# Performance work log

Hardware: AMD Instinct MI355X
Metric: run time of the kernel (lower is better)

The kernel has to match this reference:

```python
import jax, jax.numpy as jnp
import numpy as np

DIM = 512
HEADS = 2
DIM_HEAD = 64          # dim // 8
INNER = HEADS * DIM_HEAD
M = 256                # num_landmarks = dim // 2
PINV_ITERS = 6
KERNEL = 33            # residual_conv_kernel default
LN_EPS = 1e-5


def setup_inputs() -> dict:
    key = jax.random.key(0)
    ks = jax.random.split(key, 5)
    b, n = 4, 8192
    x = jax.random.normal(ks[0], (b, n, DIM), jnp.float32)
    gamma = jnp.ones((DIM,), jnp.float32)
    beta = jnp.zeros((DIM,), jnp.float32)
    w_qkv = jax.random.normal(ks[1], (DIM, 3 * INNER), jnp.float32) * 0.02
    w_out = jax.random.normal(ks[2], (INNER, DIM), jnp.float32) * 0.02
    b_out = jnp.zeros((DIM,), jnp.float32)
    w_res = jax.random.normal(ks[3], (HEADS, 1, KERNEL, 1), jnp.float32) * 0.02
    return {"x": x, "gamma": gamma, "beta": beta, "w_qkv": w_qkv,
            "w_out": w_out, "b_out": b_out, "w_res": w_res}


def moore_penrose_pinv(x, iters=PINV_ITERS):
    # x: [b, h, m, m]
    abs_x = jnp.abs(x)
    col = abs_x.sum(-1)
    row = abs_x.sum(-2)
    z = jnp.swapaxes(x, -1, -2) / (jnp.max(col) * jnp.max(row))
    I = jnp.eye(x.shape[-1], dtype=x.dtype)
    for _ in range(iters):
        xz = x @ z
        z = 0.25 * z @ (13 * I - xz @ (15 * I - xz @ (7 * I - xz)))
    return z


def reference(x, gamma, beta, w_qkv, w_out, b_out, w_res):
    b, n, d = x.shape
    # LayerNorm
    mu = x.mean(-1, keepdims=True)
    var = jnp.mean((x - mu) ** 2, axis=-1, keepdims=True)
    xn = (x - mu) / jnp.sqrt(var + LN_EPS) * gamma + beta
    # pad seq (on the left) to a multiple of M; no-op when n % M == 0
    rem = n % M
    if rem:
        xn = jnp.pad(xn, ((0, 0), (M - rem, 0), (0, 0)))
    N = xn.shape[1]
    qkv = xn @ w_qkv                        # [b, N, 3*INNER]
    q, k, v = jnp.split(qkv, 3, axis=-1)
    to_heads = lambda t: t.reshape(b, N, HEADS, DIM_HEAD).transpose(0, 2, 1, 3)
    q, k, v = to_heads(q), to_heads(k), to_heads(v)   # [b, h, N, dh]
    q = q * (DIM_HEAD ** -0.5)
    l = N // M
    q_l = q.reshape(b, HEADS, M, l, DIM_HEAD).mean(3)  # [b, h, M, dh]
    k_l = k.reshape(b, HEADS, M, l, DIM_HEAD).mean(3)
    sim1 = jnp.einsum('bhid,bhjd->bhij', q, k_l)       # [b, h, N, M]
    sim2 = jnp.einsum('bhid,bhjd->bhij', q_l, k_l)     # [b, h, M, M]
    sim3 = jnp.einsum('bhid,bhjd->bhij', q_l, k)       # [b, h, M, N]
    a1 = jax.nn.softmax(sim1, axis=-1)
    a2 = jax.nn.softmax(sim2, axis=-1)
    a3 = jax.nn.softmax(sim3, axis=-1)
    a2_inv = moore_penrose_pinv(a2)
    out = (a1 @ a2_inv) @ (a3 @ v)                     # [b, h, N, dh]
    # depthwise residual conv over sequence dim of v
    res = jax.lax.conv_general_dilated(
        v, w_res, window_strides=(1, 1),
        padding=[(KERNEL // 2, KERNEL // 2), (0, 0)],
        dimension_numbers=('NCHW', 'OIHW', 'NCHW'),
        feature_group_count=HEADS)
    out = out + res
    out = out.transpose(0, 2, 1, 3).reshape(b, N, INNER)
    out = out @ w_out + b_out
    out = out[:, -n:]
    return x + out
```

## Files before the change

kernel.cpp:

```cpp
#include <hip/hip_runtime.h>
#include <math.h>


#define BB 4
#define HH 2
#define NSEQ 8192
#define DMODEL 512
#define DH 64
#define MLAND 256
#define LCH 32
#define W3 384
#define INNER 128
#define KER 33
#define BH (BB*HH)

typedef __attribute__((ext_vector_type(8))) short short8v;
typedef __attribute__((ext_vector_type(4))) short short4v;
typedef __attribute__((ext_vector_type(4))) float f32x4;

__device__ __forceinline__ short f2bf(float f) {
    unsigned u = __float_as_uint(f);
    u = (u + 0x7FFFu + ((u >> 16) & 1u)) >> 16;
    return (short)u;
}

__global__ __launch_bounds__(256) void ln_qkv_kernel(
    const float* __restrict__ x, const float* __restrict__ gamma,
    const float* __restrict__ beta, const float* __restrict__ wqkv,
    float* __restrict__ q, float* __restrict__ k, float* __restrict__ v)
{
    __shared__ float xn[32][513];
    __shared__ float gs[512];
    __shared__ float bs[512];
    const int t = threadIdx.x;
    const int row0 = blockIdx.x * 32;

    for (int i = t; i < 512; i += 256) { gs[i] = gamma[i]; bs[i] = beta[i]; }
    __syncthreads();

    const int wave = t >> 6;
    const int lane = t & 63;
    #pragma unroll 1
    for (int i = 0; i < 8; ++i) {
        const int r = wave * 8 + i;
        const float* xr = x + (size_t)(row0 + r) * DMODEL + lane * 8;
        const float4 a = *(const float4*)(xr);
        const float4 b = *(const float4*)(xr + 4);
        float s  = a.x + a.y + a.z + a.w + b.x + b.y + b.z + b.w;
        float ss = a.x*a.x + a.y*a.y + a.z*a.z + a.w*a.w
                 + b.x*b.x + b.y*b.y + b.z*b.z + b.w*b.w;
        #pragma unroll
        for (int o = 32; o > 0; o >>= 1) {
            s  += __shfl_xor(s, o, 64);
            ss += __shfl_xor(ss, o, 64);
        }
        const float mu = s * (1.0f/512.0f);
        const float var = ss * (1.0f/512.0f) - mu*mu;
        const float rstd = rsqrtf(var + 1e-5f);
        const int c = lane * 8;
        xn[r][c+0] = (a.x - mu) * rstd * gs[c+0] + bs[c+0];
        xn[r][c+1] = (a.y - mu) * rstd * gs[c+1] + bs[c+1];
        xn[r][c+2] = (a.z - mu) * rstd * gs[c+2] + bs[c+2];
        xn[r][c+3] = (a.w - mu) * rstd * gs[c+3] + bs[c+3];
        xn[r][c+4] = (b.x - mu) * rstd * gs[c+4] + bs[c+4];
        xn[r][c+5] = (b.y - mu) * rstd * gs[c+5] + bs[c+5];
        xn[r][c+6] = (b.z - mu) * rstd * gs[c+6] + bs[c+6];
        xn[r][c+7] = (b.w - mu) * rstd * gs[c+7] + bs[c+7];
    }
    __syncthreads();

    const int c0 = (t & 63) * 6;
    const int r0 = (t >> 6) * 8;
    float acc[8][6];
    #pragma unroll
    for (int i = 0; i < 8; ++i)
        #pragma unroll
        for (int j = 0; j < 6; ++j) acc[i][j] = 0.0f;

    #pragma unroll 4
    for (int kk = 0; kk < 512; ++kk) {
        const float* wrow = wqkv + (size_t)kk * W3 + c0;
        const float w0 = wrow[0], w1 = wrow[1], w2 = wrow[2];
        const float w3 = wrow[3], w4 = wrow[4], w5 = wrow[5];
        #pragma unroll
        for (int i = 0; i < 8; ++i) {
            const float xv = xn[r0+i][kk];
            acc[i][0] = fmaf(xv, w0, acc[i][0]);
            acc[i][1] = fmaf(xv, w1, acc[i][1]);
            acc[i][2] = fmaf(xv, w2, acc[i][2]);
            acc[i][3] = fmaf(xv, w3, acc[i][3]);
            acc[i][4] = fmaf(xv, w4, acc[i][4]);
            acc[i][5] = fmaf(xv, w5, acc[i][5]);
        }
    }

    #pragma unroll
    for (int i = 0; i < 8; ++i) {
        const int grow = row0 + r0 + i;
        const int b = grow >> 13;
        const int n = grow & (NSEQ - 1);
        #pragma unroll
        for (int j = 0; j < 6; ++j) {
            const int c = c0 + j;
            const float val = acc[i][j];
            if (c < INNER) {
                const int h = c >> 6, d = c & 63;
                q[(((size_t)b*HH + h)*NSEQ + n)*DH + d] = val * 0.125f;
            } else if (c < 2*INNER) {
                const int cc = c - INNER;
                const int h = cc >> 6, d = cc & 63;
                k[(((size_t)b*HH + h)*NSEQ + n)*DH + d] = val;
            } else {
                const int cc = c - 2*INNER;
                const int h = cc >> 6, d = cc & 63;
                v[(((size_t)b*HH + h)*NSEQ + n)*DH + d] = val;
            }
        }
    }
}

__global__ __launch_bounds__(256) void landmark_kernel(
    const float* __restrict__ q, const float* __restrict__ k,
    float* __restrict__ ql, float* __restrict__ kl)
{
    const int t = threadIdx.x;
    const int g = blockIdx.x * 4 + (t >> 6);
    const int d = t & 63;
    const int bh = g >> 8;
    const int m  = g & 255;
    const float* qb = q + ((size_t)bh * NSEQ + (size_t)m * LCH) * DH + d;
    const float* kb = k + ((size_t)bh * NSEQ + (size_t)m * LCH) * DH + d;
    float sq = 0.0f, sk = 0.0f;
    #pragma unroll
    for (int i = 0; i < LCH; ++i) { sq += qb[i*DH]; sk += kb[i*DH]; }
    ql[((size_t)bh * MLAND + m) * DH + d] = sq * (1.0f/LCH);
    kl[((size_t)bh * MLAND + m) * DH + d] = sk * (1.0f/LCH);
}

__global__ __launch_bounds__(256) void sim2_kernel(
    const float* __restrict__ ql, const float* __restrict__ kl,
    float* __restrict__ a2)
{
    const int bh = blockIdx.x >> 8;
    const int i  = blockIdx.x & 255;
    const int j  = threadIdx.x;
    __shared__ float qrow[64];
    __shared__ float red[8];
    if (j < 64) qrow[j] = ql[((size_t)bh*MLAND + i)*DH + j];
    __syncthreads();
    const float4* k4 = (const float4*)(kl + ((size_t)bh*MLAND + j)*DH);
    float s = 0.0f;
    #pragma unroll
    for (int u = 0; u < 16; ++u) {
        const float4 kv = k4[u];
        s = fmaf(qrow[u*4+0], kv.x, s);
        s = fmaf(qrow[u*4+1], kv.y, s);
        s = fmaf(qrow[u*4+2], kv.z, s);
        s = fmaf(qrow[u*4+3], kv.w, s);
    }
    float m = s;
    #pragma unroll
    for (int o = 32; o > 0; o >>= 1) m = fmaxf(m, __shfl_xor(m, o, 64));
    if ((j & 63) == 0) red[j >> 6] = m;
    __syncthreads();
    m = fmaxf(fmaxf(red[0], red[1]), fmaxf(red[2], red[3]));
    const float e = __expf(s - m);
    float l = e;
    #pragma unroll
    for (int o = 32; o > 0; o >>= 1) l += __shfl_xor(l, o, 64);
    if ((j & 63) == 0) red[4 + (j >> 6)] = l;
    __syncthreads();
    l = red[4] + red[5] + red[6] + red[7];
    a2[((size_t)bh*MLAND + i)*MLAND + j] = e / l;
}

__global__ void initmax_kernel(unsigned int* mx) {
    if (threadIdx.x < 2) mx[threadIdx.x] = 0u;
}

__global__ __launch_bounds__(256) void pinv_sums_kernel(
    const float* __restrict__ a2, unsigned int* __restrict__ mx)
{
    const int bh = blockIdx.x;
    const int t = threadIdx.x;
    const float* A = a2 + (size_t)bh * MLAND * MLAND;
    float rs = 0.0f, cs = 0.0f;
    const float4* row4 = (const float4*)(A + (size_t)t * MLAND);
    #pragma unroll 8
    for (int u = 0; u < 64; ++u) {
        const float4 val = row4[u];
        rs += fabsf(val.x) + fabsf(val.y) + fabsf(val.z) + fabsf(val.w);
    }
    #pragma unroll 8
    for (int i = 0; i < MLAND; ++i) cs += fabsf(A[(size_t)i*MLAND + t]);
    __shared__ float red[8];
    float mrs = rs, mcs = cs;
    #pragma unroll
    for (int o = 32; o > 0; o >>= 1) {
        mrs = fmaxf(mrs, __shfl_xor(mrs, o, 64));
        mcs = fmaxf(mcs, __shfl_xor(mcs, o, 64));
    }
    if ((t & 63) == 0) { red[t>>6] = mrs; red[4+(t>>6)] = mcs; }
    __syncthreads();
    if (t == 0) {
        const float a = fmaxf(fmaxf(red[0],red[1]), fmaxf(red[2],red[3]));
        const float b = fmaxf(fmaxf(red[4],red[5]), fmaxf(red[6],red[7]));
        atomicMax(&mx[0], __float_as_uint(a));
        atomicMax(&mx[1], __float_as_uint(b));
    }
}

__global__ __launch_bounds__(256) void z0_kernel(
    const float* __restrict__ a2, const unsigned int* __restrict__ mx,
    float* __restrict__ z)
{
    const float scale = 1.0f / (__uint_as_float(mx[0]) * __uint_as_float(mx[1]));
    const size_t idx = (size_t)blockIdx.x * 256 + threadIdx.x;
    const size_t bh = idx >> 16;
    const size_t i = (idx >> 8) & 255;
    const size_t j = idx & 255;
    z[idx] = a2[(bh << 16) | (j << 8) | i] * scale;
}

__global__ __launch_bounds__(256) void mm256_kernel(
    float* __restrict__ C, const float* __restrict__ A,
    const float* __restrict__ Bm, float c1, float c2, int NC)
{
    __shared__ float As[32][65];
    __shared__ float Bs[64][68];
    const int bh = blockIdx.z;
    const int row0 = blockIdx.y * 32;
    const int col0 = blockIdx.x * 64;
    const float* Ab = A + (size_t)bh * MLAND * MLAND;
    const float* Bb = Bm + (size_t)bh * MLAND * NC;
    const int t = threadIdx.x;
    const int tc = (t & 15) * 4;
    const int tr = (t >> 4) * 2;
    float acc[2][4] = {{0,0,0,0},{0,0,0,0}};
    for (int k0 = 0; k0 < 256; k0 += 64) {
        #pragma unroll
        for (int u = 0; u < 2; ++u) {
            const int idx = t + u*256;
            const int r = idx >> 4, c4 = (idx & 15) * 4;
            const float4 val = *(const float4*)(Ab + (size_t)(row0 + r) * MLAND + k0 + c4);
            As[r][c4+0] = val.x; As[r][c4+1] = val.y;
            As[r][c4+2] = val.z; As[r][c4+3] = val.w;
        }
        #pragma unroll
        for (int u = 0; u < 4; ++u) {
            const int idx = t + u*256;
            const int r = idx >> 4, c4 = (idx & 15) * 4;
            *(float4*)&Bs[r][c4] = *(const float4*)(Bb + (size_t)(k0 + r) * NC + col0 + c4);
        }
        __syncthreads();
        #pragma unroll 8
        for (int kk = 0; kk < 64; ++kk) {
            const float a0 = As[tr][kk];
            const float a1 = As[tr+1][kk];
            const float4 b4 = *(const float4*)&Bs[kk][tc];
            acc[0][0] = fmaf(a0, b4.x, acc[0][0]);
            acc[0][1] = fmaf(a0, b4.y, acc[0][1]);
            acc[0][2] = fmaf(a0, b4.z, acc[0][2]);
            acc[0][3] = fmaf(a0, b4.w, acc[0][3]);
            acc[1][0] = fmaf(a1, b4.x, acc[1][0]);
            acc[1][1] = fmaf(a1, b4.y, acc[1][1]);
            acc[1][2] = fmaf(a1, b4.z, acc[1][2]);
            acc[1][3] = fmaf(a1, b4.w, acc[1][3]);
        }
        __syncthreads();
    }
    #pragma unroll
    for (int i = 0; i < 2; ++i) {
        const int r = row0 + tr + i;
        #pragma unroll
        for (int j = 0; j < 4; ++j) {
            const int c = col0 + tc + j;
            float val = c2 * acc[i][j];
            if (c1 != 0.0f) val = fmaf(c1, Ab[(size_t)r * MLAND + c], val);
            C[((size_t)bh * MLAND + r) * NC + c] = val;
        }
    }
}

__global__ __launch_bounds__(256, 1) void sim3_kernel(
    const float* __restrict__ ql, const float* __restrict__ kg,
    const float* __restrict__ vg, float* __restrict__ po,
    float* __restrict__ pm, float* __restrict__ pl)
{
    __shared__ float ks[64][68];
    __shared__ float vs[64][68];
    const int ch = blockIdx.x;
    const int bh = blockIdx.y;
    const int t = threadIdx.x;
    float4 q4[16];
    {
        const float* qr = ql + ((size_t)bh * MLAND + t) * DH;
        #pragma unroll
        for (int u = 0; u < 16; ++u) q4[u] = *(const float4*)(qr + u*4);
    }
    float4 o4[16];
    #pragma unroll
    for (int u = 0; u < 16; ++u) o4[u] = make_float4(0.f,0.f,0.f,0.f);
    float m = -1e30f, l = 0.0f;

    #pragma unroll 1
    for (int sc = 0; sc < 4; ++sc) {
        const int j0 = ch * 256 + sc * 64;
        #pragma unroll
        for (int u = 0; u < 4; ++u) {
            const int idx = t + u*256;
            const int r = idx >> 4, c4 = (idx & 15) * 4;
            *(float4*)&ks[r][c4] = *(const float4*)(kg + ((size_t)bh*NSEQ + j0 + r)*DH + c4);
            *(float4*)&vs[r][c4] = *(const float4*)(vg + ((size_t)bh*NSEQ + j0 + r)*DH + c4);
        }
        __syncthreads();
        #pragma unroll 1
        for (int b16 = 0; b16 < 4; ++b16) {
            float s[16];
            #pragma unroll
            for (int c = 0; c < 16; ++c) {
                const int cc = b16*16 + c;
                float a = 0.0f;
                #pragma unroll
                for (int u = 0; u < 16; ++u) {
                    const float4 kv = *(const float4*)&ks[cc][u*4];
                    a = fmaf(q4[u].x, kv.x, a);
                    a = fmaf(q4[u].y, kv.y, a);
                    a = fmaf(q4[u].z, kv.z, a);
                    a = fmaf(q4[u].w, kv.w, a);
                }
                s[c] = a;
            }
            float bm = s[0];
            #pragma unroll
            for (int c = 1; c < 16; ++c) bm = fmaxf(bm, s[c]);
            const float mn = fmaxf(m, bm);
            const float scale = __expf(m - mn);
            l *= scale;
            #pragma unroll
            for (int u = 0; u < 16; ++u) {
                o4[u].x *= scale; o4[u].y *= scale;
                o4[u].z *= scale; o4[u].w *= scale;
            }
            #pragma unroll
            for (int c = 0; c < 16; ++c) {
                const int cc = b16*16 + c;
                const float p = __expf(s[c] - mn);
                l += p;
                #pragma unroll
                for (int u = 0; u < 16; ++u) {
                    const float4 vv = *(const float4*)&vs[cc][u*4];
                    o4[u].x = fmaf(p, vv.x, o4[u].x);
                    o4[u].y = fmaf(p, vv.y, o4[u].y);
                    o4[u].z = fmaf(p, vv.z, o4[u].z);
                    o4[u].w = fmaf(p, vv.w, o4[u].w);
                }
            }
            m = mn;
        }
        __syncthreads();
    }
    float* od = po + (((size_t)bh*32 + ch) * MLAND + t) * DH;
    #pragma unroll
    for (int u = 0; u < 16; ++u) *(float4*)(od + u*4) = o4[u];
    pm[((size_t)bh*32 + ch) * MLAND + t] = m;
    pl[((size_t)bh*32 + ch) * MLAND + t] = l;
}

__global__ __launch_bounds__(256) void sim3red_kernel(
    const float* __restrict__ po, const float* __restrict__ pm,
    const float* __restrict__ pl, float* __restrict__ a3v)
{
    const int g = blockIdx.x * 4 + (threadIdx.x >> 6);
    const int d = threadIdx.x & 63;
    const int bh = g >> 8;
    const int r = g & 255;
    float M = -1e30f;
    #pragma unroll
    for (int c = 0; c < 32; ++c)
        M = fmaxf(M, pm[((size_t)bh*32 + c)*MLAND + r]);
    float L = 0.0f, o = 0.0f;
    #pragma unroll 1
    for (int c = 0; c < 32; ++c) {
        const float w = __expf(pm[((size_t)bh*32 + c)*MLAND + r] - M);
        L = fmaf(pl[((size_t)bh*32 + c)*MLAND + r], w, L);
        o = fmaf(po[(((size_t)bh*32 + c)*MLAND + r)*DH + d], w, o);
    }
    a3v[((size_t)bh*MLAND + r)*DH + d] = o / L;
}

__global__ __launch_bounds__(256) void packkl_kernel(
    const float* __restrict__ klm, short* __restrict__ klb)
{
    const int idx = blockIdx.x * 256 + threadIdx.x;
    klb[idx] = f2bf(klm[idx]);
}

__global__ __launch_bounds__(256) void packwt_kernel(
    const float* __restrict__ Wm, short* __restrict__ wtb)
{
    const int idx = blockIdx.x * 256 + threadIdx.x;
    const int bh = idx >> 14;
    const int rem = idx & 16383;
    const int d = rem >> 8;
    const int m = rem & 255;
    wtb[idx] = f2bf(Wm[((size_t)bh * MLAND + m) * DH + d]);
}

__global__ __launch_bounds__(256, 2) void final1_mfma_kernel(
    const float* __restrict__ q, const short* __restrict__ klb,
    const short* __restrict__ wtb, float* __restrict__ inner)
{
    __shared__ short ldsA[16384];
    __shared__ short ldsW[16384];
    const int bh = blockIdx.y;
    const int b = bh >> 1;
    const int h = bh & 1;
    const int t = threadIdx.x;
    const int w = t >> 6;
    const int l = t & 63;
    const int lr = l & 15;
    const int lg = l >> 4;

    {
        const short* klsrc = klb + (size_t)bh * 16384;
        const short* wtsrc = wtb + (size_t)bh * 16384;
        #pragma unroll
        for (int u = 0; u < 8; ++u) {
            const int gi = t + u * 256;
            const int m  = gi >> 3, sl = gi & 7;
            *(short8v*)&ldsA[m*64 + (sl ^ (m & 7))*8] =
                *(const short8v*)(klsrc + gi*8);
            const int dd = gi >> 5, sw = gi & 31;
            *(short8v*)&ldsW[dd*256 + (sw ^ (dd & 7))*8] =
                *(const short8v*)(wtsrc + gi*8);
        }
    }
    __syncthreads();

    const int n = blockIdx.x * 64 + w * 16 + lr;
    short8v qb0, qb1;
    {
        const float* qr = q + ((size_t)bh * NSEQ + n) * DH + lg * 8;
        const float4 f0 = *(const float4*)qr;
        const float4 f1 = *(const float4*)(qr + 4);
        const float4 f2 = *(const float4*)(qr + 32);
        const float4 f3 = *(const float4*)(qr + 36);
        qb0[0]=f2bf(f0.x); qb0[1]=f2bf(f0.y); qb0[2]=f2bf(f0.z); qb0[3]=f2bf(f0.w);
        qb0[4]=f2bf(f1.x); qb0[5]=f2bf(f1.y); qb0[6]=f2bf(f1.z); qb0[7]=f2bf(f1.w);
        qb1[0]=f2bf(f2.x); qb1[1]=f2bf(f2.y); qb1[2]=f2bf(f2.z); qb1[3]=f2bf(f2.w);
        qb1[4]=f2bf(f3.x); qb1[5]=f2bf(f3.y); qb1[6]=f2bf(f3.z); qb1[7]=f2bf(f3.w);
    }

    f32x4 accS[16];
    #pragma unroll
    for (int mt = 0; mt < 16; ++mt) accS[mt] = (f32x4){0.f,0.f,0.f,0.f};
    const int s8 = lr & 7;
    #pragma unroll
    for (int mt = 0; mt < 16; ++mt) {
        const int m = mt * 16 + lr;
        const short8v a0 = *(const short8v*)&ldsA[m*64 + ((0*4 + lg) ^ s8)*8];
        const short8v a1 = *(const short8v*)&ldsA[m*64 + ((1*4 + lg) ^ s8)*8];
        accS[mt] = __builtin_amdgcn_mfma_f32_16x16x32_bf16(a0, qb0, accS[mt], 0, 0, 0);
        accS[mt] = __builtin_amdgcn_mfma_f32_16x16x32_bf16(a1, qb1, accS[mt], 0, 0, 0);
    }

    float mloc = -1e30f;
    #pragma unroll
    for (int mt = 0; mt < 16; ++mt)
        #pragma unroll
        for (int j = 0; j < 4; ++j) mloc = fmaxf(mloc, accS[mt][j]);
    mloc = fmaxf(mloc, __shfl_xor(mloc, 16, 64));
    mloc = fmaxf(mloc, __shfl_xor(mloc, 32, 64));
    float lsum = 0.0f;
    #pragma unroll
    for (int mt = 0; mt < 16; ++mt)
        #pragma unroll
        for (int j = 0; j < 4; ++j) {
            const float p = __expf(accS[mt][j] - mloc);
            accS[mt][j] = p;
            lsum += p;
        }
    lsum += __shfl_xor(lsum, 16, 64);
    lsum += __shfl_xor(lsum, 32, 64);

    __syncthreads();

    {
        short* pw = ldsA + w * 4096;
        #pragma unroll
        for (int mt = 0; mt < 16; ++mt) {
            short4v pk;
            pk[0] = f2bf(accS[mt][0]); pk[1] = f2bf(accS[mt][1]);
            pk[2] = f2bf(accS[mt][2]); pk[3] = f2bf(accS[mt][3]);
            const int byteoff = (mt*32 + lg*8) ^ (s8 << 4);
            *(short4v*)&pw[lr*256 + (byteoff >> 1)] = pk;
        }
    }
    __syncthreads();

    short8v pb[8];
    {
        const short* pw = ldsA + w * 4096;
        #pragma unroll
        for (int kc = 0; kc < 8; ++kc) {
            const int byteoff = (kc*64 + lg*16) ^ (s8 << 4);
            pb[kc] = *(const short8v*)&pw[lr*256 + (byteoff >> 1)];
        }
    }
    f32x4 accO[4];
    #pragma unroll
    for (int dt = 0; dt < 4; ++dt) accO[dt] = (f32x4){0.f,0.f,0.f,0.f};
    #pragma unroll
    for (int dt = 0; dt < 4; ++dt) {
        const int d = dt * 16 + lr;
        #pragma unroll
        for (int kc = 0; kc < 8; ++kc) {
            const short8v wa = *(const short8v*)&ldsW[d*256 + (((kc*64 + lg*16) ^ (s8 << 4)) >> 1)];
            accO[dt] = __builtin_amdgcn_mfma_f32_16x16x32_bf16(wa, pb[kc], accO[dt], 0, 0, 0);
        }
    }

    const float rl = 1.0f / lsum;
    float* ob = inner + ((size_t)b * NSEQ + n) * INNER + h * DH + lg * 4;
    #pragma unroll
    for (int dt = 0; dt < 4; ++dt) {
        float4 o;
        o.x = accO[dt][0] * rl; o.y = accO[dt][1] * rl;
        o.z = accO[dt][2] * rl; o.w = accO[dt][3] * rl;
        *(float4*)(ob + dt * 16) = o;
    }
}

__global__ __launch_bounds__(256) void conv_add_kernel(
    const float* __restrict__ vg, const float* __restrict__ wres,
    float* __restrict__ inner)
{
    __shared__ float wr[KER];
    const int bh = blockIdx.y;
    const int b = bh >> 1;
    const int h = bh & 1;
    const int t = threadIdx.x;
    if (t < KER) wr[t] = wres[h*KER + t];
    __syncthreads();
    const int d = t & 63;
    const int g = t >> 6;
    const int n0 = blockIdx.x * 128;
    #pragma unroll 1
    for (int i = 0; i < 32; ++i) {
        const int n = n0 + g + i*4;
        float acc = 0.0f;
        #pragma unroll
        for (int tt = 0; tt < KER; ++tt) {
            const int nn = n - 16 + tt;
            if (nn >= 0 && nn < NSEQ)
                acc = fmaf(vg[((size_t)bh*NSEQ + nn)*DH + d], wr[tt], acc);
        }
        const size_t idx = ((size_t)b*NSEQ + n)*INNER + h*DH + d;
        inner[idx] += acc;
    }
}

__global__ __launch_bounds__(256) void final2_kernel(
    const float* __restrict__ inner, const float* __restrict__ wout,
    const float* __restrict__ bout, const float* __restrict__ x,
    float* __restrict__ out)
{
    __shared__ float is[32][129];
    const int t = threadIdx.x;
    const size_t row0 = (size_t)blockIdx.x * 32;
    #pragma unroll
    for (int u = 0; u < 4; ++u) {
        const int idx = t + u*256;
        const int r = idx >> 5, c4 = (idx & 31) * 4;
        const float4 val = *(const float4*)(inner + (row0 + r)*INNER + c4);
        is[r][c4+0]=val.x; is[r][c4+1]=val.y; is[r][c4+2]=val.z; is[r][c4+3]=val.w;
    }
    __syncthreads();
    const int c0 = (t & 63) * 8;
    const int r0 = (t >> 6) * 8;
    float acc[8][8];
    #pragma unroll
    for (int i = 0; i < 8; ++i)
        #pragma unroll
        for (int j = 0; j < 8; ++j) acc[i][j] = 0.0f;
    #pragma unroll 2
    for (int kk = 0; kk < 128; ++kk) {
        const float4 w0 = *(const float4*)(wout + (size_t)kk*DMODEL + c0);
        const float4 w1 = *(const float4*)(wout + (size_t)kk*DMODEL + c0 + 4);
        #pragma unroll
        for (int i = 0; i < 8; ++i) {
            const float xv = is[r0+i][kk];
            acc[i][0] = fmaf(xv, w0.x, acc[i][0]);
            acc[i][1] = fmaf(xv, w0.y, acc[i][1]);
            acc[i][2] = fmaf(xv, w0.z, acc[i][2]);
            acc[i][3] = fmaf(xv, w0.w, acc[i][3]);
            acc[i][4] = fmaf(xv, w1.x, acc[i][4]);
            acc[i][5] = fmaf(xv, w1.y, acc[i][5]);
            acc[i][6] = fmaf(xv, w1.z, acc[i][6]);
            acc[i][7] = fmaf(xv, w1.w, acc[i][7]);
        }
    }
    const float4 b0 = *(const float4*)(bout + c0);
    const float4 b1 = *(const float4*)(bout + c0 + 4);
    #pragma unroll
    for (int i = 0; i < 8; ++i) {
        const size_t row = row0 + r0 + i;
        const float4 x0 = *(const float4*)(x + row*DMODEL + c0);
        const float4 x1 = *(const float4*)(x + row*DMODEL + c0 + 4);
        float4 o0, o1;
        o0.x = acc[i][0] + b0.x + x0.x;
        o0.y = acc[i][1] + b0.y + x0.y;
        o0.z = acc[i][2] + b0.z + x0.z;
        o0.w = acc[i][3] + b0.w + x0.w;
        o1.x = acc[i][4] + b1.x + x1.x;
        o1.y = acc[i][5] + b1.y + x1.y;
        o1.z = acc[i][6] + b1.z + x1.z;
        o1.w = acc[i][7] + b1.w + x1.w;
        *(float4*)(out + row*DMODEL + c0) = o0;
        *(float4*)(out + row*DMODEL + c0 + 4) = o1;
    }
}

extern "C" void kernel_launch(void* const* d_in, const int* in_sizes, int n_in,
                              void* d_out, int out_size, void* d_ws, size_t ws_size,
                              hipStream_t stream)
{
    const float* x     = (const float*)d_in[0];
    const float* gamma = (const float*)d_in[1];
    const float* beta  = (const float*)d_in[2];
    const float* wqkv  = (const float*)d_in[3];
    const float* wout  = (const float*)d_in[4];
    const float* bout  = (const float*)d_in[5];
    const float* wres  = (const float*)d_in[6];
    float* out = (float*)d_out;

    float* ws = (float*)d_ws;
    const size_t QS = (size_t)BH * NSEQ * DH;
    const size_t LS = (size_t)BH * MLAND * DH;
    const size_t MS = (size_t)BH * MLAND * MLAND;
    float* q    = ws;
    float* kbuf = q + QS;
    float* vbuf = kbuf + QS;
    float* ql   = vbuf + QS;
    float* klm  = ql + LS;
    float* a2   = klm + LS;
    float* zA   = a2 + MS;
    float* zB   = zA + MS;
    float* xz   = zB + MS;
    float* t1   = xz + MS;
    float* t2   = t1 + MS;
    float* a3v  = t2 + MS;
    float* Wm   = a3v + LS;
    float* po   = Wm + LS;
    float* pm   = po + QS;
    float* pl   = pm + (size_t)BH * 32 * MLAND;
    unsigned int* mx = (unsigned int*)(pl + (size_t)BH * 32 * MLAND);
    float* inner = po;
    short* klb = (short*)kbuf;
    short* wtb = (short*)kbuf + LS;

    ln_qkv_kernel<<<(BB*NSEQ)/32, 256, 0, stream>>>(x, gamma, beta, wqkv, q, kbuf, vbuf);
    landmark_kernel<<<(BH*MLAND)/4, 256, 0, stream>>>(q, kbuf, ql, klm);
    sim2_kernel<<<BH*MLAND, 256, 0, stream>>>(ql, klm, a2);

    sim3_kernel<<<dim3(32, BH), 256, 0, stream>>>(ql, kbuf, vbuf, po, pm, pl);
    sim3red_kernel<<<(BH*MLAND)/4, 256, 0, stream>>>(po, pm, pl, a3v);

    initmax_kernel<<<1, 64, 0, stream>>>(mx);
    pinv_sums_kernel<<<BH, 256, 0, stream>>>(a2, mx);
    z0_kernel<<<(unsigned)(MS/256), 256, 0, stream>>>(a2, mx, zA);
    float* za = zA;
    float* zb = zB;
    for (int it = 0; it < 6; ++it) {
        mm256_kernel<<<dim3(4,8,BH), 256, 0, stream>>>(xz, a2, za, 0.0f, 1.0f, 256);
        mm256_kernel<<<dim3(4,8,BH), 256, 0, stream>>>(t1, xz, xz, 7.0f, -1.0f, 256);
        mm256_kernel<<<dim3(4,8,BH), 256, 0, stream>>>(t2, xz, t1, 15.0f, -1.0f, 256);
        mm256_kernel<<<dim3(4,8,BH), 256, 0, stream>>>(zb, za, t2, 3.25f, -0.25f, 256);
        float* tmp = za; za = zb; zb = tmp;
    }
    mm256_kernel<<<dim3(1,8,BH), 256, 0, stream>>>(Wm, za, a3v, 0.0f, 1.0f, 64);

    packkl_kernel<<<(unsigned)(LS/256), 256, 0, stream>>>(klm, klb);
    packwt_kernel<<<(unsigned)(LS/256), 256, 0, stream>>>(Wm, wtb);

    final1_mfma_kernel<<<dim3(NSEQ/64, BH), 256, 0, stream>>>(q, klb, wtb, inner);
    conv_add_kernel<<<dim3(NSEQ/128, BH), 256, 0, stream>>>(vbuf, wres, inner);
    final2_kernel<<<(BB*NSEQ)/32, 256, 0, stream>>>(inner, wout, bout, x, out);
}
```

Baseline: 1.129 ms.

## Move QKV and output projections to bf16 MFMA with packed weight fragments

```diff
diff --git a/kernel.cpp b/kernel.cpp
--- a/kernel.cpp
+++ b/kernel.cpp
@@ -24,26 +24,75 @@
     return (short)u;
 }
 
-__global__ __launch_bounds__(256) void ln_qkv_kernel(
+__device__ __forceinline__ void gload_lds16(const short* g, short* l) {
+    __builtin_amdgcn_global_load_lds(
+        (const __attribute__((address_space(1))) unsigned int*)(g),
+        (__attribute__((address_space(3))) unsigned int*)(l), 16, 0, 0);
+}
+
+__global__ __launch_bounds__(256) void pack_wqkv_kernel(
+    const float* __restrict__ w, short* __restrict__ wf)
+{
+    const int idx = blockIdx.x * 256 + threadIdx.x;
+    const int l = idx & 63;
+    const int ct = (idx >> 6) % 24;
+    const int ks = idx / 1536;
+    const int c = ct * 16 + (l & 15);
+    const int k0 = ks * 32 + (l >> 4) * 8;
+    short8v o;
+    #pragma unroll
+    for (int j = 0; j < 8; ++j) o[j] = f2bf(w[(size_t)(k0 + j) * W3 + c]);
+    *(short8v*)&wf[(size_t)idx * 8] = o;
+}
+
+__global__ __launch_bounds__(256) void pack_wout_kernel(
+    const float* __restrict__ w, short* __restrict__ wf)
+{
+    const int idx = blockIdx.x * 256 + threadIdx.x;
+    const int l = idx & 63;
+    const int ct = (idx >> 6) & 31;
+    const int ks = idx >> 11;
+    const int c = ct * 16 + (l & 15);
+    const int k0 = ks * 32 + (l >> 4) * 8;
+    short8v o;
+    #pragma unroll
+    for (int j = 0; j < 8; ++j) o[j] = f2bf(w[(size_t)(k0 + j) * DMODEL + c]);
+    *(short8v*)&wf[(size_t)idx * 8] = o;
+}
+
+__global__ __launch_bounds__(256) void pack_inner_kernel(
+    const float* __restrict__ in, short* __restrict__ o)
+{
+    const size_t i8 = (size_t)blockIdx.x * 256 + threadIdx.x;
+    const float4 a = *(const float4*)(in + i8 * 8);
+    const float4 b = *(const float4*)(in + i8 * 8 + 4);
+    short8v s;
+    s[0]=f2bf(a.x); s[1]=f2bf(a.y); s[2]=f2bf(a.z); s[3]=f2bf(a.w);
+    s[4]=f2bf(b.x); s[5]=f2bf(b.y); s[6]=f2bf(b.z); s[7]=f2bf(b.w);
+    *(short8v*)&o[i8 * 8] = s;
+}
+
+__global__ __launch_bounds__(256, 1) void ln_qkv_mfma_kernel(
     const float* __restrict__ x, const float* __restrict__ gamma,
-    const float* __restrict__ beta, const float* __restrict__ wqkv,
+    const float* __restrict__ beta, const short* __restrict__ wfrag,
     float* __restrict__ q, float* __restrict__ k, float* __restrict__ v)
 {
-    __shared__ float xn[32][513];
+    __shared__ short xn[64 * 512];
+    __shared__ short bsh[2 * 12288];
     __shared__ float gs[512];
-    __shared__ float bs[512];
+    __shared__ float bs2[512];
     const int t = threadIdx.x;
-    const int row0 = blockIdx.x * 32;
-
-    for (int i = t; i < 512; i += 256) { gs[i] = gamma[i]; bs[i] = beta[i]; }
-    __syncthreads();
-
-    const int wave = t >> 6;
+    const int w = t >> 6;
     const int lane = t & 63;
+    const int row0 = blockIdx.x * 64;
+
+    for (int i = t; i < 512; i += 256) { gs[i] = gamma[i]; bs2[i] = beta[i]; }
+    __syncthreads();
+
     #pragma unroll 1
-    for (int i = 0; i < 8; ++i) {
-        const int r = wave * 8 + i;
-        const float* xr = x + (size_t)(row0 + r) * DMODEL + lane * 8;
+    for (int i = 0; i < 16; ++i) {
+        const int r = w * 16 + i;
+        const float* xr = x + ((size_t)row0 + r) * DMODEL + lane * 8;
         const float4 a = *(const float4*)(xr);
         const float4 b = *(const float4*)(xr + 4);
         float s  = a.x + a.y + a.z + a.w + b.x + b.y + b.z + b.w;
@@ -58,63 +107,68 @@
         const float var = ss * (1.0f/512.0f) - mu*mu;
         const float rstd = rsqrtf(var + 1e-5f);
         const int c = lane * 8;
-        xn[r][c+0] = (a.x - mu) * rstd * gs[c+0] + bs[c+0];
-        xn[r][c+1] = (a.y - mu) * rstd * gs[c+1] + bs[c+1];
-        xn[r][c+2] = (a.z - mu) * rstd * gs[c+2] + bs[c+2];
-        xn[r][c+3] = (a.w - mu) * rstd * gs[c+3] + bs[c+3];
-        xn[r][c+4] = (b.x - mu) * rstd * gs[c+4] + bs[c+4];
-        xn[r][c+5] = (b.y - mu) * rstd * gs[c+5] + bs[c+5];
-        xn[r][c+6] = (b.z - mu) * rstd * gs[c+6] + bs[c+6];
-        xn[r][c+7] = (b.w - mu) * rstd * gs[c+7] + bs[c+7];
-    }
-    __syncthreads();
-
-    const int c0 = (t & 63) * 6;
-    const int r0 = (t >> 6) * 8;
-    float acc[8][6];
-    #pragma unroll
-    for (int i = 0; i < 8; ++i)
-        #pragma unroll
-        for (int j = 0; j < 6; ++j) acc[i][j] = 0.0f;
-
-    #pragma unroll 4
-    for (int kk = 0; kk < 512; ++kk) {
-        const float* wrow = wqkv + (size_t)kk * W3 + c0;
-        const float w0 = wrow[0], w1 = wrow[1], w2 = wrow[2];
-        const float w3 = wrow[3], w4 = wrow[4], w5 = wrow[5];
-        #pragma unroll
-        for (int i = 0; i < 8; ++i) {
-            const float xv = xn[r0+i][kk];
-            acc[i][0] = fmaf(xv, w0, acc[i][0]);
-            acc[i][1] = fmaf(xv, w1, acc[i][1]);
-            acc[i][2] = fmaf(xv, w2, acc[i][2]);
-            acc[i][3] = fmaf(xv, w3, acc[i][3]);
-            acc[i][4] = fmaf(xv, w4, acc[i][4]);
-            acc[i][5] = fmaf(xv, w5, acc[i][5]);
-        }
-    }
-
-    #pragma unroll
-    for (int i = 0; i < 8; ++i) {
-        const int grow = row0 + r0 + i;
-        const int b = grow >> 13;
-        const int n = grow & (NSEQ - 1);
-        #pragma unroll
-        for (int j = 0; j < 6; ++j) {
-            const int c = c0 + j;
-            const float val = acc[i][j];
-            if (c < INNER) {
-                const int h = c >> 6, d = c & 63;
-                q[(((size_t)b*HH + h)*NSEQ + n)*DH + d] = val * 0.125f;
-            } else if (c < 2*INNER) {
-                const int cc = c - INNER;
-                const int h = cc >> 6, d = cc & 63;
-                k[(((size_t)b*HH + h)*NSEQ + n)*DH + d] = val;
-            } else {
-                const int cc = c - 2*INNER;
-                const int h = cc >> 6, d = cc & 63;
-                v[(((size_t)b*HH + h)*NSEQ + n)*DH + d] = val;
-            }
+        short8v o8;
+        o8[0] = f2bf((a.x - mu) * rstd * gs[c+0] + bs2[c+0]);
+        o8[1] = f2bf((a.y - mu) * rstd * gs[c+1] + bs2[c+1]);
+        o8[2] = f2bf((a.z - mu) * rstd * gs[c+2] + bs2[c+2]);
+        o8[3] = f2bf((a.w - mu) * rstd * gs[c+3] + bs2[c+3]);
+        o8[4] = f2bf((b.x - mu) * rstd * gs[c+4] + bs2[c+4]);
+        o8[5] = f2bf((b.y - mu) * rstd * gs[c+5] + bs2[c+5]);
+        o8[6] = f2bf((b.z - mu) * rstd * gs[c+6] + bs2[c+6]);
+        o8[7] = f2bf((b.w - mu) * rstd * gs[c+7] + bs2[c+7]);
+        *(short8v*)&xn[r * 512 + ((lane ^ (r & 7)) * 8)] = o8;
+    }
+
+    {
+        const short* src = wfrag + ((size_t)0 * 1536 + w * 384 + lane) * 8;
+        short* dst = &bsh[0 * 12288 + (w * 384) * 8];
+        #pragma unroll
+        for (int uu = 0; uu < 6; ++uu)
+            gload_lds16(src + uu * 512, dst + uu * 512);
+    }
+
+    f32x4 acc[24];
+    #pragma unroll
+    for (int ct = 0; ct < 24; ++ct) acc[ct] = (f32x4){0.f,0.f,0.f,0.f};
+
+    const int lr = lane & 15;
+    const int lg = lane >> 4;
+    const int arow = w * 16 + lr;
+
+    #pragma unroll 1
+    for (int ks = 0; ks < 16; ++ks) {
+        __syncthreads();
+        if (ks < 15) {
+            const int ksn = ks + 1;
+            const short* src = wfrag + ((size_t)ksn * 1536 + w * 384 + lane) * 8;
+            short* dst = &bsh[(ksn & 1) * 12288 + (w * 384) * 8];
+            #pragma unroll
+            for (int uu = 0; uu < 6; ++uu)
+                gload_lds16(src + uu * 512, dst + uu * 512);
+        }
+        const short8v af = *(const short8v*)&xn[arow * 512 + (((ks*4 + lg) ^ (arow & 7)) * 8)];
+        const short* bb = &bsh[(ks & 1) * 12288];
+        #pragma unroll
+        for (int ct = 0; ct < 24; ++ct) {
+            const short8v bf = *(const short8v*)&bb[(ct * 64 + lane) * 8];
+            acc[ct] = __builtin_amdgcn_mfma_f32_16x16x32_bf16(af, bf, acc[ct], 0, 0, 0);
+        }
+    }
+
+    #pragma unroll
+    for (int ct = 0; ct < 24; ++ct) {
+        const int c = ct * 16 + lr;
+        const int sel = c >> 7;
+        const int h = (c >> 6) & 1;
+        const int d = c & 63;
+        float* dst = (sel == 0) ? q : (sel == 1) ? k : v;
+        const float sc = (sel == 0) ? 0.125f : 1.0f;
+        #pragma unroll
+        for (int j = 0; j < 4; ++j) {
+            const int grow = row0 + w * 16 + lg * 4 + j;
+            const int b = grow >> 13;
+            const int n = grow & (NSEQ - 1);
+            dst[(((size_t)b * HH + h) * NSEQ + n) * DH + d] = acc[ct][j] * sc;
         }
     }
 }
@@ -561,64 +615,52 @@
     }
 }
 
-__global__ __launch_bounds__(256) void final2_kernel(
-    const float* __restrict__ inner, const float* __restrict__ wout,
+__global__ __launch_bounds__(256) void final2_mfma_kernel(
+    const short* __restrict__ innerb, const short* __restrict__ wfrag2,
     const float* __restrict__ bout, const float* __restrict__ x,
     float* __restrict__ out)
 {
-    __shared__ float is[32][129];
+    __shared__ short ia[64 * 128];
     const int t = threadIdx.x;
-    const size_t row0 = (size_t)blockIdx.x * 32;
+    const int w = t >> 6;
+    const int lane = t & 63;
+    const size_t row0 = (size_t)blockIdx.x * 64;
+
     #pragma unroll
     for (int u = 0; u < 4; ++u) {
-        const int idx = t + u*256;
-        const int r = idx >> 5, c4 = (idx & 31) * 4;
-        const float4 val = *(const float4*)(inner + (row0 + r)*INNER + c4);
-        is[r][c4+0]=val.x; is[r][c4+1]=val.y; is[r][c4+2]=val.z; is[r][c4+3]=val.w;
-    }
-    __syncthreads();
-    const int c0 = (t & 63) * 8;
-    const int r0 = (t >> 6) * 8;
-    float acc[8][8];
-    #pragma unroll
-    for (int i = 0; i < 8; ++i)
-        #pragma unroll
-        for (int j = 0; j < 8; ++j) acc[i][j] = 0.0f;
-    #pragma unroll 2
-    for (int kk = 0; kk < 128; ++kk) {
-        const float4 w0 = *(const float4*)(wout + (size_t)kk*DMODEL + c0);
-        const float4 w1 = *(const float4*)(wout + (size_t)kk*DMODEL + c0 + 4);
-        #pragma unroll
-        for (int i = 0; i < 8; ++i) {
-            const float xv = is[r0+i][kk];
-            acc[i][0] = fmaf(xv, w0.x, acc[i][0]);
-            acc[i][1] = fmaf(xv, w0.y, acc[i][1]);
-            acc[i][2] = fmaf(xv, w0.z, acc[i][2]);
-            acc[i][3] = fmaf(xv, w0.w, acc[i][3]);
-            acc[i][4] = fmaf(xv, w1.x, acc[i][4]);
-            acc[i][5] = fmaf(xv, w1.y, acc[i][5]);
-            acc[i][6] = fmaf(xv, w1.z, acc[i][6]);
-            acc[i][7] = fmaf(xv, w1.w, acc[i][7]);
-        }
-    }
-    const float4 b0 = *(const float4*)(bout + c0);
-    const float4 b1 = *(const float4*)(bout + c0 + 4);
-    #pragma unroll
-    for (int i = 0; i < 8; ++i) {
-        const size_t row = row0 + r0 + i;
-        const float4 x0 = *(const float4*)(x + row*DMODEL + c0);
-        const float4 x1 = *(const float4*)(x + row*DMODEL + c0 + 4);
-        float4 o0, o1;
-        o0.x = acc[i][0] + b0.x + x0.x;
-        o0.y = acc[i][1] + b0.y + x0.y;
-        o0.z = acc[i][2] + b0.z + x0.z;
-        o0.w = acc[i][3] + b0.w + x0.w;
-        o1.x = acc[i][4] + b1.x + x1.x;
-        o1.y = acc[i][5] + b1.y + x1.y;
-        o1.z = acc[i][6] + b1.z + x1.z;
-        o1.w = acc[i][7] + b1.w + x1.w;
-        *(float4*)(out + row*DMODEL + c0) = o0;
-        *(float4*)(out + row*DMODEL + c0 + 4) = o1;
+        const int idx = u * 256 + t;
+        const int r = idx >> 4, sl = idx & 15;
+        *(short8v*)&ia[r * 128 + ((sl ^ (r & 7)) * 8)] =
+            *(const short8v*)&innerb[(row0 + r) * 128 + sl * 8];
+    }
+    __syncthreads();
+
+    const int lr = lane & 15;
+    const int lg = lane >> 4;
+    const int arow = w * 16 + lr;
+    f32x4 acc[32];
+    #pragma unroll
+    for (int ct = 0; ct < 32; ++ct) acc[ct] = (f32x4){0.f,0.f,0.f,0.f};
+
+    #pragma unroll
+    for (int ks = 0; ks < 4; ++ks) {
+        const short8v af = *(const short8v*)&ia[arow * 128 + (((ks*4 + lg) ^ (arow & 7)) * 8)];
+        #pragma unroll
+        for (int ct = 0; ct < 32; ++ct) {
+            const short8v bf = *(const short8v*)&wfrag2[((size_t)(ks*32 + ct)*64 + lane) * 8];
+            acc[ct] = __builtin_amdgcn_mfma_f32_16x16x32_bf16(af, bf, acc[ct], 0, 0, 0);
+        }
+    }
+
+    #pragma unroll
+    for (int ct = 0; ct < 32; ++ct) {
+        const int c = ct * 16 + lr;
+        const float bo = bout[c];
+        #pragma unroll
+        for (int j = 0; j < 4; ++j) {
+            const size_t row = row0 + w * 16 + lg * 4 + j;
+            out[row * DMODEL + c] = acc[ct][j] + bo + x[row * DMODEL + c];
+        }
     }
 }
 
@@ -659,8 +701,12 @@
     float* inner = po;
     short* klb = (short*)kbuf;
     short* wtb = (short*)kbuf + LS;
-
-    ln_qkv_kernel<<<(BB*NSEQ)/32, 256, 0, stream>>>(x, gamma, beta, wqkv, q, kbuf, vbuf);
+    short* wfrag  = (short*)pm;
+    short* wfrag2 = (short*)a3v;
+    short* innerb = (short*)q;
+
+    pack_wqkv_kernel<<<96, 256, 0, stream>>>(wqkv, wfrag);
+    ln_qkv_mfma_kernel<<<512, 256, 0, stream>>>(x, gamma, beta, wfrag, q, kbuf, vbuf);
     landmark_kernel<<<(BH*MLAND)/4, 256, 0, stream>>>(q, kbuf, ql, klm);
     sim2_kernel<<<BH*MLAND, 256, 0, stream>>>(ql, klm, a2);
 
@@ -681,10 +727,12 @@
     }
     mm256_kernel<<<dim3(1,8,BH), 256, 0, stream>>>(Wm, za, a3v, 0.0f, 1.0f, 64);
 
+    pack_wout_kernel<<<32, 256, 0, stream>>>(wout, wfrag2);
     packkl_kernel<<<(unsigned)(LS/256), 256, 0, stream>>>(klm, klb);
     packwt_kernel<<<(unsigned)(LS/256), 256, 0, stream>>>(Wm, wtb);
 
     final1_mfma_kernel<<<dim3(NSEQ/64, BH), 256, 0, stream>>>(q, klb, wtb, inner);
     conv_add_kernel<<<dim3(NSEQ/128, BH), 256, 0, stream>>>(vbuf, wres, inner);
-    final2_kernel<<<(BB*NSEQ)/32, 256, 0, stream>>>(inner, wout, bout, x, out);
-}
+    pack_inner_kernel<<<2048, 256, 0, stream>>>(inner, innerb);
+    final2_mfma_kernel<<<512, 256, 0, stream>>>(innerb, wfrag2, bout, x, out);
+}
```

Result: faster. 989.9 us (-12.3%).
